# Kernel optimization log

Hardware: AMD Instinct MI355X
Metric: run time of the kernel (lower is better)

The kernel has to match this reference:

```python
import jax, jax.numpy as jnp
import numpy as np

EMBED_DIM = 1024
NUM_HEADS = 16
WINDOW = 128  # one-sided window length w; total span 2w+1


def setup_inputs() -> dict:
    key = jax.random.key(0)
    ks = jax.random.split(key, 9)
    D = EMBED_DIM
    x = jax.random.normal(ks[0], (2, 8192, D), dtype=jnp.float32)
    s = 0.02
    Wq = jax.random.normal(ks[1], (D, D), dtype=jnp.float32) * s
    bq = jax.random.normal(ks[2], (D,), dtype=jnp.float32) * s
    Wk = jax.random.normal(ks[3], (D, D), dtype=jnp.float32) * s
    bk = jax.random.normal(ks[4], (D,), dtype=jnp.float32) * s
    Wv = jax.random.normal(ks[5], (D, D), dtype=jnp.float32) * s
    bv = jax.random.normal(ks[6], (D,), dtype=jnp.float32) * s
    Wo = jax.random.normal(ks[7], (D, D), dtype=jnp.float32) * s
    bo = jax.random.normal(ks[8], (D,), dtype=jnp.float32) * s
    return {"x": x, "Wq": Wq, "bq": bq, "Wk": Wk, "bk": bk,
            "Wv": Wv, "bv": bv, "Wo": Wo, "bo": bo}


def _sliding_window_attention(x, Wq, bq, Wk, bk, Wv, bv, Wo, bo):
    B, S, D = x.shape
    H, w = NUM_HEADS, WINDOW
    hd = D // H
    bs = w            # block size = window_length; 3 blocks cover [i-w, i+w]
    nb = S // bs

    def proj(W, b):
        y = x @ W.T + b                              # torch Linear: x @ W.T + b
        return y.reshape(B, S, H, hd).transpose(0, 2, 1, 3)  # [B,H,S,hd]

    q = proj(Wq, bq)
    k = proj(Wk, bk)
    v = proj(Wv, bv)

    qb = q.reshape(B, H, nb, bs, hd)
    # pad K/V with one zero block on each side, then build 3-block contexts
    pad = ((0, 0), (0, 0), (bs, bs), (0, 0))
    kp = jnp.pad(k, pad).reshape(B, H, nb + 2, bs, hd)
    vp = jnp.pad(v, pad).reshape(B, H, nb + 2, bs, hd)
    k_ctx = jnp.concatenate([kp[:, :, :-2], kp[:, :, 1:-1], kp[:, :, 2:]], axis=3)  # [B,H,nb,3bs,hd]
    v_ctx = jnp.concatenate([vp[:, :, :-2], vp[:, :, 1:-1], vp[:, :, 2:]], axis=3)

    scale = 1.0 / np.sqrt(hd).astype(np.float32)
    scores = jnp.einsum('bhnqd,bhnkd->bhnqk', qb, k_ctx) * scale  # [B,H,nb,bs,3bs]

    # band mask: |k_pos - q_pos| <= w, and k_pos in [0, S)
    q_off = jnp.arange(bs)
    k_off = jnp.arange(3 * bs)
    rel = k_off[None, :] - bs - q_off[:, None]                # [bs,3bs]
    win_ok = jnp.abs(rel) <= w
    k_pos = (jnp.arange(nb)[:, None, None] - 1) * bs + k_off[None, None, :]
    valid = (k_pos >= 0) & (k_pos < S)                        # [nb,1,3bs]
    mask = win_ok[None] & valid                               # [nb,bs,3bs]

    scores = jnp.where(mask[None, None], scores, jnp.float32(-jnp.inf))
    weights = jax.nn.softmax(scores, axis=-1)

    out = jnp.einsum('bhnqk,bhnkd->bhnqd', weights, v_ctx)    # [B,H,nb,bs,hd]
    out = out.reshape(B, H, S, hd).transpose(0, 2, 1, 3).reshape(B, S, D)
    return out @ Wo.T + bo


def reference(x, Wq, bq, Wk, bk, Wv, bv, Wo, bo):
    return _sliding_window_attention(x, Wq, bq, Wk, bk, Wv, bv, Wo, bo)
```

## Files before the change

kernel.cpp:

```cpp
#include <hip/hip_runtime.h>

typedef __attribute__((ext_vector_type(4))) float f32x4;
typedef __attribute__((ext_vector_type(8))) short s16x8;

#define MFMA16(a, b, c) __builtin_amdgcn_mfma_f32_16x16x32_bf16((a), (b), (c), 0, 0, 0)

__device__ __forceinline__ unsigned short f2bf_bits(float f) {
  unsigned int u = __float_as_uint(f);
  unsigned int r = (u + 0x7fffu + ((u >> 16) & 1u)) >> 16;
  return (unsigned short)r;
}

__device__ __forceinline__ void gl_lds16(const void* g, void* l) {
  __builtin_amdgcn_global_load_lds((const __attribute__((address_space(1))) void*)g,
                                   (__attribute__((address_space(3))) void*)l, 16, 0, 0);
}

__global__ __launch_bounds__(256) void f2bf_kernel(const float* __restrict__ in,
                                                   unsigned short* __restrict__ out, int n4) {
  int idx = blockIdx.x * 256 + threadIdx.x;
  int stride = gridDim.x * 256;
  for (int i = idx; i < n4; i += stride) {
    float4 v = ((const float4*)in)[i];
    ushort4 o;
    o.x = f2bf_bits(v.x); o.y = f2bf_bits(v.y);
    o.z = f2bf_bits(v.z); o.w = f2bf_bits(v.w);
    ((ushort4*)out)[i] = o;
  }
}

__global__ __launch_bounds__(256) void f2bf_w4(const float* __restrict__ w0,
                                               const float* __restrict__ w1,
                                               const float* __restrict__ w2,
                                               const float* __restrict__ w3,
                                               unsigned short* __restrict__ o0,
                                               unsigned short* __restrict__ o1,
                                               unsigned short* __restrict__ o2,
                                               unsigned short* __restrict__ o3) {
  const int s = blockIdx.y;
  const float* in = (s == 0) ? w0 : (s == 1) ? w1 : (s == 2) ? w2 : w3;
  unsigned short* out = (s == 0) ? o0 : (s == 1) ? o1 : (s == 2) ? o2 : o3;
  int i = blockIdx.x * 256 + threadIdx.x;
  float4 v = ((const float4*)in)[i];
  ushort4 o;
  o.x = f2bf_bits(v.x); o.y = f2bf_bits(v.y);
  o.z = f2bf_bits(v.z); o.w = f2bf_bits(v.w);
  ((ushort4*)out)[i] = o;
}

#define GEMM_CORE64(A_, B_, K_)                                                       \
  f32x4 acc[4][4];                                                                    \
  _Pragma("unroll") for (int i = 0; i < 4; ++i)                                       \
      _Pragma("unroll") for (int j = 0; j < 4; ++j)                                   \
          acc[i][j] = (f32x4){0.f, 0.f, 0.f, 0.f};                                    \
  {                                                                                   \
    const int rb = tid >> 3;                                                          \
    const int cb = (((tid & 7) ^ (rb & 7))) * 8;                                      \
    _Pragma("unroll 1") for (int k0 = 0; k0 < (K_); k0 += 64) {                       \
      _Pragma("unroll") for (int i = 0; i < 4; ++i) {                                 \
        gl_lds16((A_) + (size_t)(rb + 32 * i) * (K_) + k0 + cb, &Al[(tid + 256 * i) * 8]); \
        gl_lds16((B_) + (size_t)(rb + 32 * i) * (K_) + k0 + cb, &Bl[(tid + 256 * i) * 8]); \
      }                                                                               \
      __syncthreads();                                                                \
      _Pragma("unroll") for (int ks = 0; ks < 2; ++ks) {                              \
        s16x8 af[4], bfr[4];                                                          \
        const int pch = ((ks * 4 + quad) ^ (l15 & 7)) * 8;                            \
        _Pragma("unroll") for (int i = 0; i < 4; ++i)                                 \
            af[i] = *(const s16x8*)&Al[(wm + i * 16 + l15) * 64 + pch];               \
        _Pragma("unroll") for (int j = 0; j < 4; ++j)                                 \
            bfr[j] = *(const s16x8*)&Bl[(wn + j * 16 + l15) * 64 + pch];              \
        _Pragma("unroll") for (int i = 0; i < 4; ++i)                                 \
            _Pragma("unroll") for (int j = 0; j < 4; ++j)                             \
                acc[i][j] = MFMA16(af[i], bfr[j], acc[i][j]);                         \
      }                                                                               \
      __syncthreads();                                                                \
    }                                                                                 \
  }

__global__ __launch_bounds__(256) void gemm_qkv(const unsigned short* __restrict__ A,
                                                const unsigned short* __restrict__ Wq,
                                                const unsigned short* __restrict__ Wk,
                                                const unsigned short* __restrict__ Wv,
                                                const float* __restrict__ bq,
                                                const float* __restrict__ bk,
                                                const float* __restrict__ bv,
                                                unsigned short* __restrict__ Qo,
                                                unsigned short* __restrict__ Ko,
                                                unsigned short* __restrict__ Vt) {
  __shared__ unsigned short Al[128 * 64];
  __shared__ unsigned short Bl[128 * 64];
  const int tid = threadIdx.x;
  const int lane = tid & 63, wave = tid >> 6;
  const int l15 = lane & 15, quad = lane >> 4;
  const int wm = (wave >> 1) * 64, wn = (wave & 1) * 64;
  const int bx = blockIdx.x;
  const int sel = blockIdx.y >> 3;
  const int by = blockIdx.y & 7;
  const int K = 1024, N = 1024;

  const unsigned short* W = (sel == 0) ? Wq : (sel == 1) ? Wk : Wv;
  const float* bias = (sel == 0) ? bq : (sel == 1) ? bk : bv;

  const unsigned short* Abase = A + (size_t)bx * 128 * K;
  const unsigned short* Bbase = W + (size_t)by * 128 * K;

  GEMM_CORE64(Abase, Bbase, K)

#pragma unroll
  for (int j = 0; j < 4; ++j) {
    const int cn = by * 128 + wn + j * 16 + l15;
    const float bj = bias[cn];
#pragma unroll
    for (int i = 0; i < 4; ++i) {
      const int r0 = bx * 128 + wm + i * 16 + quad * 4;
#pragma unroll
      for (int r = 0; r < 4; ++r) {
        const int row = r0 + r;
        const float v = acc[i][j][r] + bj;
        if (sel == 0) {
          Qo[(size_t)row * N + cn] = f2bf_bits(v);
        } else if (sel == 1) {
          Ko[(size_t)row * N + cn] = f2bf_bits(v);
        } else {
          Vt[((size_t)(row >> 13) * 1024 + cn) * 8192 + (row & 8191)] = f2bf_bits(v);
        }
      }
    }
  }
}

__global__ __launch_bounds__(256) void gemm_out(const unsigned short* __restrict__ A,
                                                const unsigned short* __restrict__ B,
                                                const float* __restrict__ bias,
                                                float* __restrict__ Cf) {
  __shared__ unsigned short Al[128 * 64];
  __shared__ unsigned short Bl[128 * 64];
  const int tid = threadIdx.x;
  const int lane = tid & 63, wave = tid >> 6;
  const int l15 = lane & 15, quad = lane >> 4;
  const int wm = (wave >> 1) * 64, wn = (wave & 1) * 64;
  const int bx = blockIdx.x, by = blockIdx.y;
  const int K = 1024, N = 1024;

  const unsigned short* Abase = A + (size_t)bx * 128 * K;
  const unsigned short* Bbase = B + (size_t)by * 128 * K;

  GEMM_CORE64(Abase, Bbase, K)

#pragma unroll
  for (int j = 0; j < 4; ++j) {
    const int cn = by * 128 + wn + j * 16 + l15;
    const float bj = bias[cn];
#pragma unroll
    for (int i = 0; i < 4; ++i) {
      const int r0 = bx * 128 + wm + i * 16 + quad * 4;
#pragma unroll
      for (int r = 0; r < 4; ++r) Cf[(size_t)(r0 + r) * N + cn] = acc[i][j][r] + bj;
    }
  }
}

__global__ __launch_bounds__(256, 3) void attn_kernel(const unsigned short* __restrict__ Q,
                                                      const unsigned short* __restrict__ Km,
                                                      const unsigned short* __restrict__ Vt,
                                                      unsigned short* __restrict__ O) {
  const int n = blockIdx.x;
  const int bh = blockIdx.y;
  const int b = bh >> 4, h = bh & 15;
  const int tid = threadIdx.x, lane = tid & 63, wave = tid >> 6;
  const int l15 = lane & 15, quad = lane >> 4;

  __shared__ unsigned short Kl[384 * 64];
  __shared__ unsigned short Ps[4][16 * 40];

  const int base_row = n * 128 - 128;

  for (int i = 0; i < 12; ++i) {
    const int c = i * 256 + tid;
    const int row = c >> 3;
    const int qc = (c & 7) ^ (row & 7);
    int gr = base_row + row;
    gr = min(max(gr, 0), 8191);
    gl_lds16(Km + (size_t)(b * 8192 + gr) * 1024 + h * 64 + qc * 8, &Kl[c * 8]);
  }
  __syncthreads();

  const unsigned short* Vbase = Vt + (size_t)bh * 64 * 8192;
  unsigned short* strip = &Ps[wave][0];

  for (int mt = 0; mt < 2; ++mt) {
    const int qt = wave * 2 + mt;
    const int q0 = n * 128 + qt * 16;
    const int qp = q0 + l15;

    const unsigned short* qptr = Q + (size_t)(b * 8192 + qp) * 1024 + h * 64 + quad * 8;
    const s16x8 bq0 = *(const s16x8*)qptr;
    const s16x8 bq1 = *(const s16x8*)(qptr + 32);

    f32x4 o[4];
#pragma unroll
    for (int dt = 0; dt < 4; ++dt) o[dt] = (f32x4){0.f, 0.f, 0.f, 0.f};
    float lsum = 0.f;

    const int krel0 = qt * 16;

#pragma unroll 1
    for (int p = 0; p < 9; ++p) {
      f32x4 st[2];
#pragma unroll
      for (int tt = 0; tt < 2; ++tt) {
        int rel = krel0 + p * 32 + tt * 16 + l15;
        int rr = min(rel, 383);
        const int ro = rr * 8;
        const int sw = rr & 7;
        const s16x8 ka0 = *(const s16x8*)&Kl[(ro + (quad ^ sw)) * 8];
        const s16x8 ka1 = *(const s16x8*)&Kl[(ro + ((4 + quad) ^ sw)) * 8];
        f32x4 a = (f32x4){0.f, 0.f, 0.f, 0.f};
        a = MFMA16(ka0, bq0, a);
        a = MFMA16(ka1, bq1, a);
        st[tt] = a;
      }
      ushort4 w0, w1;
#pragma unroll
      for (int tt = 0; tt < 2; ++tt) {
        unsigned short* wp = tt ? (unsigned short*)&w1 : (unsigned short*)&w0;
#pragma unroll
        for (int r = 0; r < 4; ++r) {
          const int kp = base_row + krel0 + p * 32 + tt * 16 + quad * 4 + r;
          const int dd = kp - qp;
          const bool ok = (kp >= 0) && (kp < 8192) && (dd >= -128) && (dd <= 128);
          const float pv = ok ? __expf(st[tt][r] * 0.125f) : 0.f;
          lsum += pv;
          wp[r] = f2bf_bits(pv);
        }
      }
      *(ushort4*)&strip[l15 * 40 + quad * 4] = w0;
      *(ushort4*)&strip[l15 * 40 + 16 + quad * 4] = w1;
      const s16x8 pf = *(const s16x8*)&strip[l15 * 40 + quad * 8];
      int kc = base_row + krel0 + p * 32 + quad * 8;
      kc = min(max(kc, 0), 8184);
#pragma unroll
      for (int dt = 0; dt < 4; ++dt) {
        const s16x8 va = *(const s16x8*)(Vbase + (size_t)(dt * 16 + l15) * 8192 + kc);
        o[dt] = MFMA16(va, pf, o[dt]);
      }
    }

    lsum += __shfl_xor(lsum, 16, 64);
    lsum += __shfl_xor(lsum, 32, 64);
    const float rinv = 1.f / lsum;
    unsigned short* obase = O + (size_t)(b * 8192 + qp) * 1024 + h * 64;
#pragma unroll
    for (int dt = 0; dt < 4; ++dt) {
      ushort4 w;
      unsigned short* wp = (unsigned short*)&w;
#pragma unroll
      for (int r = 0; r < 4; ++r) wp[r] = f2bf_bits(o[dt][r] * rinv);
      *(ushort4*)(obase + dt * 16 + quad * 4) = w;
    }
  }
}

extern "C" void kernel_launch(void* const* d_in, const int* in_sizes, int n_in, void* d_out,
                              int out_size, void* d_ws, size_t ws_size, hipStream_t stream) {
  const float* x = (const float*)d_in[0];
  const float* Wq = (const float*)d_in[1];
  const float* bq = (const float*)d_in[2];
  const float* Wk = (const float*)d_in[3];
  const float* bk = (const float*)d_in[4];
  const float* Wv = (const float*)d_in[5];
  const float* bv = (const float*)d_in[6];
  const float* Wo = (const float*)d_in[7];
  const float* bo = (const float*)d_in[8];
  float* out = (float*)d_out;

  const int M = 16384, D = 1024;

  unsigned short* xb = (unsigned short*)d_ws;
  unsigned short* qb = xb + (size_t)M * D;
  unsigned short* kb = qb + (size_t)M * D;
  unsigned short* vt = kb + (size_t)M * D;
  unsigned short* ab = vt + (size_t)M * D;
  unsigned short* wqb = ab + (size_t)M * D;
  unsigned short* wkb = wqb + (size_t)D * D;
  unsigned short* wvb = wkb + (size_t)D * D;
  unsigned short* wob = wvb + (size_t)D * D;

  f2bf_kernel<<<16384, 256, 0, stream>>>(x, xb, M * D / 4);
  f2bf_w4<<<dim3(1024, 4), 256, 0, stream>>>(Wq, Wk, Wv, Wo, wqb, wkb, wvb, wob);

  gemm_qkv<<<dim3(M / 128, 24), 256, 0, stream>>>(xb, wqb, wkb, wvb, bq, bk, bv, qb, kb, vt);

  attn_kernel<<<dim3(64, 32), 256, 0, stream>>>(qb, kb, vt, ab);

  gemm_out<<<dim3(M / 128, D / 128), 256, 0, stream>>>(ab, wob, bo, out);
}
```

Baseline: 443.9 us.

## Shrink GEMM tiles, fold softmax scale into Q, specialize and pipeline attention

Switches both projection GEMMs from 128x128 to 128x64 tiles with an occupancy hint of 5 blocks per CU, which doubles the grid and lowers LDS and register use per block. The 1/sqrt(hd) scale is now applied to Q in the QKV epilogue instead of inside the attention exp. The attention kernel is templated into interior and edge variants, so interior blocks use simple triangular masks without bounds clamps. V fragments are prefetched one step ahead to overlap global loads with MFMA work. The cost is two attention launches and more GEMM blocks, each doing less work.

```diff
diff --git a/kernel.cpp b/kernel.cpp
--- a/kernel.cpp
+++ b/kernel.cpp
@@ -48,67 +48,70 @@
   ((ushort4*)out)[i] = o;
 }
 
-#define GEMM_CORE64(A_, B_, K_)                                                       \
-  f32x4 acc[4][4];                                                                    \
+#define GEMM_CORE_128x64(A_, B_, K_)                                                  \
+  f32x4 acc[4][2];                                                                    \
   _Pragma("unroll") for (int i = 0; i < 4; ++i)                                       \
-      _Pragma("unroll") for (int j = 0; j < 4; ++j)                                   \
+      _Pragma("unroll") for (int j = 0; j < 2; ++j)                                   \
           acc[i][j] = (f32x4){0.f, 0.f, 0.f, 0.f};                                    \
   {                                                                                   \
     const int rb = tid >> 3;                                                          \
-    const int cb = (((tid & 7) ^ (rb & 7))) * 8;                                      \
+    const int cb = ((tid & 7) ^ (rb & 7)) * 8;                                        \
     _Pragma("unroll 1") for (int k0 = 0; k0 < (K_); k0 += 64) {                       \
-      _Pragma("unroll") for (int i = 0; i < 4; ++i) {                                 \
-        gl_lds16((A_) + (size_t)(rb + 32 * i) * (K_) + k0 + cb, &Al[(tid + 256 * i) * 8]); \
-        gl_lds16((B_) + (size_t)(rb + 32 * i) * (K_) + k0 + cb, &Bl[(tid + 256 * i) * 8]); \
-      }                                                                               \
+      _Pragma("unroll") for (int i = 0; i < 4; ++i)                                   \
+          gl_lds16((A_) + (size_t)(rb + 32 * i) * (K_) + k0 + cb,                     \
+                   &Al[(tid + 256 * i) * 8]);                                         \
+      _Pragma("unroll") for (int i = 0; i < 2; ++i)                                   \
+          gl_lds16((B_) + (size_t)(rb + 32 * i) * (K_) + k0 + cb,                     \
+                   &Bl[(tid + 256 * i) * 8]);                                         \
       __syncthreads();                                                                \
       _Pragma("unroll") for (int ks = 0; ks < 2; ++ks) {                              \
-        s16x8 af[4], bfr[4];                                                          \
+        s16x8 af[4], bfr[2];                                                          \
         const int pch = ((ks * 4 + quad) ^ (l15 & 7)) * 8;                            \
         _Pragma("unroll") for (int i = 0; i < 4; ++i)                                 \
             af[i] = *(const s16x8*)&Al[(wm + i * 16 + l15) * 64 + pch];               \
-        _Pragma("unroll") for (int j = 0; j < 4; ++j)                                 \
+        _Pragma("unroll") for (int j = 0; j < 2; ++j)                                 \
             bfr[j] = *(const s16x8*)&Bl[(wn + j * 16 + l15) * 64 + pch];              \
         _Pragma("unroll") for (int i = 0; i < 4; ++i)                                 \
-            _Pragma("unroll") for (int j = 0; j < 4; ++j)                             \
+            _Pragma("unroll") for (int j = 0; j < 2; ++j)                             \
                 acc[i][j] = MFMA16(af[i], bfr[j], acc[i][j]);                         \
       }                                                                               \
       __syncthreads();                                                                \
     }                                                                                 \
   }
 
-__global__ __launch_bounds__(256) void gemm_qkv(const unsigned short* __restrict__ A,
-                                                const unsigned short* __restrict__ Wq,
-                                                const unsigned short* __restrict__ Wk,
-                                                const unsigned short* __restrict__ Wv,
-                                                const float* __restrict__ bq,
-                                                const float* __restrict__ bk,
-                                                const float* __restrict__ bv,
-                                                unsigned short* __restrict__ Qo,
-                                                unsigned short* __restrict__ Ko,
-                                                unsigned short* __restrict__ Vt) {
+__global__ __launch_bounds__(256, 5) void gemm_qkv(const unsigned short* __restrict__ A,
+                                                   const unsigned short* __restrict__ Wq,
+                                                   const unsigned short* __restrict__ Wk,
+                                                   const unsigned short* __restrict__ Wv,
+                                                   const float* __restrict__ bq,
+                                                   const float* __restrict__ bk,
+                                                   const float* __restrict__ bv,
+                                                   unsigned short* __restrict__ Qo,
+                                                   unsigned short* __restrict__ Ko,
+                                                   unsigned short* __restrict__ Vt) {
   __shared__ unsigned short Al[128 * 64];
-  __shared__ unsigned short Bl[128 * 64];
+  __shared__ unsigned short Bl[64 * 64];
   const int tid = threadIdx.x;
   const int lane = tid & 63, wave = tid >> 6;
   const int l15 = lane & 15, quad = lane >> 4;
-  const int wm = (wave >> 1) * 64, wn = (wave & 1) * 64;
+  const int wm = (wave >> 1) * 64, wn = (wave & 1) * 32;
   const int bx = blockIdx.x;
-  const int sel = blockIdx.y >> 3;
-  const int by = blockIdx.y & 7;
+  const int sel = blockIdx.y >> 4;
+  const int by = blockIdx.y & 15;
   const int K = 1024, N = 1024;
 
   const unsigned short* W = (sel == 0) ? Wq : (sel == 1) ? Wk : Wv;
   const float* bias = (sel == 0) ? bq : (sel == 1) ? bk : bv;
 
   const unsigned short* Abase = A + (size_t)bx * 128 * K;
-  const unsigned short* Bbase = W + (size_t)by * 128 * K;
-
-  GEMM_CORE64(Abase, Bbase, K)
-
-#pragma unroll
-  for (int j = 0; j < 4; ++j) {
-    const int cn = by * 128 + wn + j * 16 + l15;
+  const unsigned short* Bbase = W + (size_t)by * 64 * K;
+
+  GEMM_CORE_128x64(Abase, Bbase, K)
+
+  const float qs = (sel == 0) ? 0.125f : 1.0f;
+#pragma unroll
+  for (int j = 0; j < 2; ++j) {
+    const int cn = by * 64 + wn + j * 16 + l15;
     const float bj = bias[cn];
 #pragma unroll
     for (int i = 0; i < 4; ++i) {
@@ -117,39 +120,38 @@
       for (int r = 0; r < 4; ++r) {
         const int row = r0 + r;
         const float v = acc[i][j][r] + bj;
-        if (sel == 0) {
-          Qo[(size_t)row * N + cn] = f2bf_bits(v);
-        } else if (sel == 1) {
-          Ko[(size_t)row * N + cn] = f2bf_bits(v);
+        if (sel == 2) {
+          Vt[((size_t)(row >> 13) * 1024 + cn) * 8192 + (row & 8191)] = f2bf_bits(v);
         } else {
-          Vt[((size_t)(row >> 13) * 1024 + cn) * 8192 + (row & 8191)] = f2bf_bits(v);
+          unsigned short* O = sel ? Ko : Qo;
+          O[(size_t)row * N + cn] = f2bf_bits(v * qs);
         }
       }
     }
   }
 }
 
-__global__ __launch_bounds__(256) void gemm_out(const unsigned short* __restrict__ A,
-                                                const unsigned short* __restrict__ B,
-                                                const float* __restrict__ bias,
-                                                float* __restrict__ Cf) {
+__global__ __launch_bounds__(256, 5) void gemm_out(const unsigned short* __restrict__ A,
+                                                   const unsigned short* __restrict__ B,
+                                                   const float* __restrict__ bias,
+                                                   float* __restrict__ Cf) {
   __shared__ unsigned short Al[128 * 64];
-  __shared__ unsigned short Bl[128 * 64];
+  __shared__ unsigned short Bl[64 * 64];
   const int tid = threadIdx.x;
   const int lane = tid & 63, wave = tid >> 6;
   const int l15 = lane & 15, quad = lane >> 4;
-  const int wm = (wave >> 1) * 64, wn = (wave & 1) * 64;
+  const int wm = (wave >> 1) * 64, wn = (wave & 1) * 32;
   const int bx = blockIdx.x, by = blockIdx.y;
   const int K = 1024, N = 1024;
 
   const unsigned short* Abase = A + (size_t)bx * 128 * K;
-  const unsigned short* Bbase = B + (size_t)by * 128 * K;
-
-  GEMM_CORE64(Abase, Bbase, K)
-
-#pragma unroll
-  for (int j = 0; j < 4; ++j) {
-    const int cn = by * 128 + wn + j * 16 + l15;
+  const unsigned short* Bbase = B + (size_t)by * 64 * K;
+
+  GEMM_CORE_128x64(Abase, Bbase, K)
+
+#pragma unroll
+  for (int j = 0; j < 2; ++j) {
+    const int cn = by * 64 + wn + j * 16 + l15;
     const float bj = bias[cn];
 #pragma unroll
     for (int i = 0; i < 4; ++i) {
@@ -160,11 +162,75 @@
   }
 }
 
+template <int MM>
+__device__ __forceinline__ void attn_step(int p, int base_row, int krel0, int qp, int quad,
+                                          int l15, const unsigned short* __restrict__ Kl,
+                                          const s16x8& bq0, const s16x8& bq1,
+                                          unsigned short* __restrict__ strip,
+                                          const unsigned short* __restrict__ Vbase,
+                                          f32x4 (&o)[4], float& lsum, s16x8 (&vf)[4]) {
+  f32x4 st[2];
+#pragma unroll
+  for (int tt = 0; tt < 2; ++tt) {
+    const int rel = krel0 + p * 32 + tt * 16 + l15;
+    const int sw = rel & 7;
+    const s16x8 ka0 = *(const s16x8*)&Kl[(rel * 8 + (quad ^ sw)) * 8];
+    const s16x8 ka1 = *(const s16x8*)&Kl[(rel * 8 + ((4 + quad) ^ sw)) * 8];
+    f32x4 a = (f32x4){0.f, 0.f, 0.f, 0.f};
+    a = MFMA16(ka0, bq0, a);
+    a = MFMA16(ka1, bq1, a);
+    st[tt] = a;
+  }
+  s16x8 vn[4];
+  if (MM != 2) {
+    int kc = base_row + krel0 + (p + 1) * 32 + quad * 8;
+    if (MM == 3) kc = max(kc, 0);
+    kc = min(kc, 8184);
+#pragma unroll
+    for (int dt = 0; dt < 4; ++dt)
+      vn[dt] = *(const s16x8*)(Vbase + (size_t)(dt * 16 + l15) * 8192 + kc);
+  }
+  ushort4 w0, w1;
+#pragma unroll
+  for (int tt = 0; tt < 2; ++tt) {
+    unsigned short* wp = tt ? (unsigned short*)&w1 : (unsigned short*)&w0;
+#pragma unroll
+    for (int r = 0; r < 4; ++r) {
+      const int c = tt * 16 + quad * 4 + r;
+      float pv;
+      if (MM == 0) {
+        pv = __expf(st[tt][r]);
+      } else if (MM == 1) {
+        pv = (c >= l15) ? __expf(st[tt][r]) : 0.f;
+      } else if (MM == 2) {
+        pv = (c <= l15) ? __expf(st[tt][r]) : 0.f;
+      } else {
+        const int kp = base_row + krel0 + p * 32 + c;
+        const bool ok = ((unsigned)(p * 32 + c - l15) <= 256u) && (kp >= 0) && (kp < 8192);
+        pv = ok ? __expf(st[tt][r]) : 0.f;
+      }
+      lsum += pv;
+      wp[r] = f2bf_bits(pv);
+    }
+  }
+  *(ushort4*)&strip[l15 * 40 + quad * 4] = w0;
+  *(ushort4*)&strip[l15 * 40 + 16 + quad * 4] = w1;
+  const s16x8 pf = *(const s16x8*)&strip[l15 * 40 + quad * 8];
+#pragma unroll
+  for (int dt = 0; dt < 4; ++dt) o[dt] = MFMA16(vf[dt], pf, o[dt]);
+  if (MM != 2) {
+#pragma unroll
+    for (int dt = 0; dt < 4; ++dt) vf[dt] = vn[dt];
+  }
+}
+
+template <bool EDGE>
 __global__ __launch_bounds__(256, 3) void attn_kernel(const unsigned short* __restrict__ Q,
                                                       const unsigned short* __restrict__ Km,
                                                       const unsigned short* __restrict__ Vt,
-                                                      unsigned short* __restrict__ O) {
-  const int n = blockIdx.x;
+                                                      unsigned short* __restrict__ O,
+                                                      int n_mul, int n_off) {
+  const int n = blockIdx.x * n_mul + n_off;
   const int bh = blockIdx.y;
   const int b = bh >> 4, h = bh & 15;
   const int tid = threadIdx.x, lane = tid & 63, wave = tid >> 6;
@@ -180,7 +246,7 @@
     const int row = c >> 3;
     const int qc = (c & 7) ^ (row & 7);
     int gr = base_row + row;
-    gr = min(max(gr, 0), 8191);
+    if (EDGE) gr = min(max(gr, 0), 8191);
     gl_lds16(Km + (size_t)(b * 8192 + gr) * 1024 + h * 64 + qc * 8, &Kl[c * 8]);
   }
   __syncthreads();
@@ -190,8 +256,8 @@
 
   for (int mt = 0; mt < 2; ++mt) {
     const int qt = wave * 2 + mt;
-    const int q0 = n * 128 + qt * 16;
-    const int qp = q0 + l15;
+    const int qp = n * 128 + qt * 16 + l15;
+    const int krel0 = qt * 16;
 
     const unsigned short* qptr = Q + (size_t)(b * 8192 + qp) * 1024 + h * 64 + quad * 8;
     const s16x8 bq0 = *(const s16x8*)qptr;
@@ -202,48 +268,25 @@
     for (int dt = 0; dt < 4; ++dt) o[dt] = (f32x4){0.f, 0.f, 0.f, 0.f};
     float lsum = 0.f;
 
-    const int krel0 = qt * 16;
-
+    s16x8 vf[4];
+    {
+      int kc = base_row + krel0 + quad * 8;
+      if (EDGE) kc = min(max(kc, 0), 8184);
+#pragma unroll
+      for (int dt = 0; dt < 4; ++dt)
+        vf[dt] = *(const s16x8*)(Vbase + (size_t)(dt * 16 + l15) * 8192 + kc);
+    }
+
+    if (EDGE) {
 #pragma unroll 1
-    for (int p = 0; p < 9; ++p) {
-      f32x4 st[2];
-#pragma unroll
-      for (int tt = 0; tt < 2; ++tt) {
-        int rel = krel0 + p * 32 + tt * 16 + l15;
-        int rr = min(rel, 383);
-        const int ro = rr * 8;
-        const int sw = rr & 7;
-        const s16x8 ka0 = *(const s16x8*)&Kl[(ro + (quad ^ sw)) * 8];
-        const s16x8 ka1 = *(const s16x8*)&Kl[(ro + ((4 + quad) ^ sw)) * 8];
-        f32x4 a = (f32x4){0.f, 0.f, 0.f, 0.f};
-        a = MFMA16(ka0, bq0, a);
-        a = MFMA16(ka1, bq1, a);
-        st[tt] = a;
-      }
-      ushort4 w0, w1;
-#pragma unroll
-      for (int tt = 0; tt < 2; ++tt) {
-        unsigned short* wp = tt ? (unsigned short*)&w1 : (unsigned short*)&w0;
-#pragma unroll
-        for (int r = 0; r < 4; ++r) {
-          const int kp = base_row + krel0 + p * 32 + tt * 16 + quad * 4 + r;
-          const int dd = kp - qp;
-          const bool ok = (kp >= 0) && (kp < 8192) && (dd >= -128) && (dd <= 128);
-          const float pv = ok ? __expf(st[tt][r] * 0.125f) : 0.f;
-          lsum += pv;
-          wp[r] = f2bf_bits(pv);
-        }
-      }
-      *(ushort4*)&strip[l15 * 40 + quad * 4] = w0;
-      *(ushort4*)&strip[l15 * 40 + 16 + quad * 4] = w1;
-      const s16x8 pf = *(const s16x8*)&strip[l15 * 40 + quad * 8];
-      int kc = base_row + krel0 + p * 32 + quad * 8;
-      kc = min(max(kc, 0), 8184);
-#pragma unroll
-      for (int dt = 0; dt < 4; ++dt) {
-        const s16x8 va = *(const s16x8*)(Vbase + (size_t)(dt * 16 + l15) * 8192 + kc);
-        o[dt] = MFMA16(va, pf, o[dt]);
-      }
+      for (int p = 0; p < 9; ++p)
+        attn_step<3>(p, base_row, krel0, qp, quad, l15, Kl, bq0, bq1, strip, Vbase, o, lsum, vf);
+    } else {
+      attn_step<1>(0, base_row, krel0, qp, quad, l15, Kl, bq0, bq1, strip, Vbase, o, lsum, vf);
+#pragma unroll 1
+      for (int p = 1; p < 8; ++p)
+        attn_step<0>(p, base_row, krel0, qp, quad, l15, Kl, bq0, bq1, strip, Vbase, o, lsum, vf);
+      attn_step<2>(8, base_row, krel0, qp, quad, l15, Kl, bq0, bq1, strip, Vbase, o, lsum, vf);
     }
 
     lsum += __shfl_xor(lsum, 16, 64);
@@ -289,9 +332,10 @@
   f2bf_kernel<<<16384, 256, 0, stream>>>(x, xb, M * D / 4);
   f2bf_w4<<<dim3(1024, 4), 256, 0, stream>>>(Wq, Wk, Wv, Wo, wqb, wkb, wvb, wob);
 
-  gemm_qkv<<<dim3(M / 128, 24), 256, 0, stream>>>(xb, wqb, wkb, wvb, bq, bk, bv, qb, kb, vt);
-
-  attn_kernel<<<dim3(64, 32), 256, 0, stream>>>(qb, kb, vt, ab);
-
-  gemm_out<<<dim3(M / 128, D / 128), 256, 0, stream>>>(ab, wob, bo, out);
-}
+  gemm_qkv<<<dim3(M / 128, 48), 256, 0, stream>>>(xb, wqb, wkb, wvb, bq, bk, bv, qb, kb, vt);
+
+  attn_kernel<false><<<dim3(62, 32), 256, 0, stream>>>(qb, kb, vt, ab, 1, 1);
+  attn_kernel<true><<<dim3(2, 32), 256, 0, stream>>>(qb, kb, vt, ab, 63, 0);
+
+  gemm_out<<<dim3(M / 128, D / 64), 256, 0, stream>>>(ab, wob, bo, out);
+}
```

Result: no change. 444.3 us (+0.1%).
